# Kernel optimization log

Hardware: AMD Instinct MI355X
Metric: run time of the kernel (lower is better)

The kernel has to match this reference:

```python
import jax, jax.numpy as jnp
import numpy as np

N = 100000
E = 1600000
B = 64
NUM_CLASSES = 10


def setup_inputs() -> dict:
    key = jax.random.key(0)
    ks = jax.random.split(key, 8)
    x = jax.random.normal(ks[0], (N, 5), dtype=jnp.float32)
    edge_index = jax.random.randint(ks[1], (2, E), 0, N, dtype=jnp.int64)
    batch = jnp.sort(jax.random.randint(ks[2], (N,), 0, B, dtype=jnp.int64))

    def glorot(k, fan_in, fan_out):
        s = jnp.sqrt(6.0 / (fan_in + fan_out)).astype(jnp.float32)
        return jax.random.uniform(k, (fan_in, fan_out), jnp.float32, -s, s)

    dims = [(5, 32), (32, 64), (64, 128), (128, 256)]
    Ws = [glorot(jax.random.fold_in(ks[3], i), a, b) for i, (a, b) in enumerate(dims)]
    bs = [jnp.zeros((b,), jnp.float32) for (_, b) in dims]
    fc1_w = glorot(ks[4], 256, 100)
    fc1_b = jnp.zeros((100,), jnp.float32)
    fc2_w = glorot(ks[5], 100, NUM_CLASSES)
    fc2_b = jnp.zeros((NUM_CLASSES,), jnp.float32)
    return {
        'x': x, 'edge_index': edge_index, 'batch': batch,
        'W1': Ws[0], 'b1': bs[0], 'W2': Ws[1], 'b2': bs[1],
        'W3': Ws[2], 'b3': bs[2], 'W4': Ws[3], 'b4': bs[3],
        'fc1_w': fc1_w, 'fc1_b': fc1_b, 'fc2_w': fc2_w, 'fc2_b': fc2_b,
    }


def _gcn_conv(x, W, b, src, dst, dinv):
    h = x @ W                                   # [N, out]
    norm = (dinv[src] * dinv[dst])[:, None]      # [E, 1]
    msg = h[src] * norm                          # gather + scale
    agg = jax.ops.segment_sum(msg, dst, num_segments=N)
    agg = agg + h * (dinv * dinv)[:, None]       # self-loop contribution
    return agg + b


def reference(x, edge_index, batch, W1, b1, W2, b2, W3, b3, W4, b4,
              fc1_w, fc1_b, fc2_w, fc2_b):
    src, dst = edge_index[0], edge_index[1]
    # degree including self-loop
    deg = jax.ops.segment_sum(jnp.ones((E,), jnp.float32), dst, num_segments=N) + 1.0
    dinv = jax.lax.rsqrt(deg)

    h = jax.nn.relu(_gcn_conv(x, W1, b1, src, dst, dinv))
    # mesh_unpool with pool target 0 -> identity
    h = jax.nn.relu(_gcn_conv(h, W2, b2, src, dst, dinv))
    h = jax.nn.relu(_gcn_conv(h, W3, b3, src, dst, dinv))
    h = jax.nn.relu(_gcn_conv(h, W4, b4, src, dst, dinv))

    # global mean pool over graphs
    sums = jax.ops.segment_sum(h, batch, num_segments=B)
    cnt = jax.ops.segment_sum(jnp.ones((N,), jnp.float32), batch, num_segments=B)
    pooled = sums / jnp.maximum(cnt, 1.0)[:, None]

    h = jax.nn.relu(pooled @ fc1_w + fc1_b)
    return jax.nn.log_softmax(h @ fc2_w + fc2_b, axis=-1)
```

## Files before the change

### kernel.cpp

```cpp
#include <hip/hip_runtime.h>
#include <hip/hip_bf16.h>
#include <cmath>

#define NN 100000
#define NE 1600000
#define NBATCH 64
#define NB 391
#define NBP 512
#define BCAP 5120
#define NPAD (NB * BCAP)

typedef __attribute__((ext_vector_type(8))) _Float16 f16x8;
typedef __attribute__((ext_vector_type(4))) float f32x4;
typedef __attribute__((ext_vector_type(2))) float f32x2;

__device__ __forceinline__ void atomAdd(float* p, float v) {
  unsafeAtomicAdd(p, v);
}

__device__ __forceinline__ unsigned char f2fp8(float f) {
  int pk = __builtin_amdgcn_cvt_pk_fp8_f32(f, f, 0, false);
  return (unsigned char)(pk & 0xff);
}

__device__ __forceinline__ void fp8x16_to_f16(uint4 v, _Float16* h) {
  f32x2 t;
  t = __builtin_amdgcn_cvt_pk_f32_fp8(v.x, false); h[0] = (_Float16)t.x;  h[1] = (_Float16)t.y;
  t = __builtin_amdgcn_cvt_pk_f32_fp8(v.x, true);  h[2] = (_Float16)t.x;  h[3] = (_Float16)t.y;
  t = __builtin_amdgcn_cvt_pk_f32_fp8(v.y, false); h[4] = (_Float16)t.x;  h[5] = (_Float16)t.y;
  t = __builtin_amdgcn_cvt_pk_f32_fp8(v.y, true);  h[6] = (_Float16)t.x;  h[7] = (_Float16)t.y;
  t = __builtin_amdgcn_cvt_pk_f32_fp8(v.z, false); h[8] = (_Float16)t.x;  h[9] = (_Float16)t.y;
  t = __builtin_amdgcn_cvt_pk_f32_fp8(v.z, true);  h[10] = (_Float16)t.x; h[11] = (_Float16)t.y;
  t = __builtin_amdgcn_cvt_pk_f32_fp8(v.w, false); h[12] = (_Float16)t.x; h[13] = (_Float16)t.y;
  t = __builtin_amdgcn_cvt_pk_f32_fp8(v.w, true);  h[14] = (_Float16)t.x; h[15] = (_Float16)t.y;
}

__global__ __launch_bounds__(256) void k_bin(const int* __restrict__ src,
    const int* __restrict__ dst, int* __restrict__ bucketCnt, unsigned* __restrict__ pairs,
    const float* __restrict__ W2, const float* __restrict__ W3, const float* __restrict__ W4,
    _Float16* __restrict__ Wt2, _Float16* __restrict__ Wt3, _Float16* __restrict__ Wt4) {
  __shared__ int hist[NBP];
  __shared__ int scn[NBP];
  __shared__ int ofs[NBP];
  __shared__ int gbase[NBP];
  __shared__ unsigned buf[4096];
  __shared__ unsigned short bufb[4096];
  const int base = blockIdx.x * 4096;
  const int n = (NE - base < 4096) ? NE - base : 4096;
  for (int i = threadIdx.x; i < NBP; i += 256) hist[i] = 0;
  __syncthreads();

  int myS[16], myD[16];
  int nloc = 0;
  for (int i = threadIdx.x, j = 0; i < n; i += 256, ++j) {
    myS[j] = src[base + i];
    myD[j] = dst[base + i];
    atomicAdd(&hist[myD[j] >> 8], 1);
    nloc = j + 1;
  }
  __syncthreads();

  scn[threadIdx.x] = hist[threadIdx.x];
  scn[threadIdx.x + 256] = hist[threadIdx.x + 256];
  __syncthreads();
  for (int off = 1; off < NBP; off <<= 1) {
    const int i0 = threadIdx.x, i1 = threadIdx.x + 256;
    int t0 = (i0 >= off) ? scn[i0 - off] : 0;
    int t1 = (i1 >= off) ? scn[i1 - off] : 0;
    __syncthreads();
    scn[i0] += t0;
    scn[i1] += t1;
    __syncthreads();
  }
  ofs[threadIdx.x] = scn[threadIdx.x] - hist[threadIdx.x];
  ofs[threadIdx.x + 256] = scn[threadIdx.x + 256] - hist[threadIdx.x + 256];
  for (int b = threadIdx.x; b < NB; b += 256) {
    int c = hist[b];
    if (c) gbase[b] = b * BCAP + atomicAdd(&bucketCnt[b], c);
  }
  __syncthreads();

  for (int j = 0; j < nloc; ++j) {
    int b = myD[j] >> 8;
    int slot = atomicAdd(&ofs[b], 1);
    buf[slot] = ((unsigned)myS[j] << 8) | ((unsigned)myD[j] & 255u);
    bufb[slot] = (unsigned short)b;
  }
  __syncthreads();

  for (int i = threadIdx.x; i < n; i += 256) {
    int b = (int)bufb[i];
    int ex = scn[b] - hist[b];
    pairs[gbase[b] + (i - ex)] = buf[i];
  }

  int idx = blockIdx.x * 256 + threadIdx.x;
  if (idx < 2048) {
    int k = idx / 64, m = idx - k * 64;
    Wt2[m * 32 + k] = (_Float16)W2[idx];
  } else if (idx < 10240) {
    int j = idx - 2048;
    int k = j / 128, m = j - k * 128;
    Wt3[m * 64 + k] = (_Float16)W3[j];
  } else if (idx < 43008) {
    int j = idx - 10240;
    int k = j / 256, m = j - k * 256;
    Wt4[m * 128 + k] = (_Float16)W4[j];
  }
}

__global__ __launch_bounds__(256) void k_cntfill(const unsigned* __restrict__ pairs,
    const int* __restrict__ bucketCnt, const int* __restrict__ batch,
    const float* __restrict__ x, int* __restrict__ rowbeg, int* __restrict__ rowend,
    float* __restrict__ dinv, int* __restrict__ csrc, float* __restrict__ pcnt,
    _Float16* __restrict__ xs8) {
  __shared__ int c[256];
  __shared__ int scn[256];
  __shared__ int rowb[256];
  __shared__ int ofs[256];
  __shared__ int h[64];
  const int tid = threadIdx.x;
  c[tid] = 0; ofs[tid] = 0;
  if (tid < 64) h[tid] = 0;
  __syncthreads();
  const int b = blockIdx.x;
  const int s = b * BCAP;
  const int e = s + bucketCnt[b];
  for (int i = s + tid; i < e; i += 256) atomicAdd(&c[pairs[i] & 255u], 1);
  __syncthreads();
  const int v = c[tid];
  scn[tid] = v;
  __syncthreads();
  for (int off = 1; off < 256; off <<= 1) {
    int t = (tid >= off) ? scn[tid - off] : 0;
    __syncthreads();
    scn[tid] += t;
    __syncthreads();
  }
  rowb[tid] = s + scn[tid] - v;
  const int node = b * 256 + tid;
  rowbeg[node] = rowb[tid];
  rowend[node] = rowb[tid] + v;
  if (node < NN) {
    const float di = rsqrtf((float)v + 1.0f);
    dinv[node] = di;
    f16x8 o = {0, 0, 0, 0, 0, 0, 0, 0};
    o[0] = (_Float16)(x[(size_t)node * 5 + 0] * di);
    o[1] = (_Float16)(x[(size_t)node * 5 + 1] * di);
    o[2] = (_Float16)(x[(size_t)node * 5 + 2] * di);
    o[3] = (_Float16)(x[(size_t)node * 5 + 3] * di);
    o[4] = (_Float16)(x[(size_t)node * 5 + 4] * di);
    *(f16x8*)(xs8 + (size_t)node * 8) = o;
    atomicAdd(&h[batch[node]], 1);
  }
  __syncthreads();
  for (int i = s + tid; i < e; i += 256) {
    unsigned p = pairs[i];
    int t = (int)(p & 255u);
    int pos = rowb[t] + atomicAdd(&ofs[t], 1);
    csrc[pos] = (int)(p >> 8);
  }
  if (tid < 64 && h[tid]) atomAdd(&pcnt[tid], (float)h[tid]);
}

struct MegaArgs {
  const _Float16* xs8;
  const int* rowbeg; const int* rowend; const int* csrc;
  const float* dinv;
  const float* W1; const float* b1;
  unsigned char* F0;
  const _Float16* Wt2; const float* b2;
  unsigned char* F1;
  const _Float16* Wt3; const float* b3;
  unsigned char* F2;
  const _Float16* Wt4; const float* b4;
  unsigned char* AG8;
  const int* batch; float* pooled; const float* pcnt;
  const float* fc1w; const float* fc1b; const float* fc2w; const float* fc2b;
  float* out;
};

__global__ __launch_bounds__(256) void kw_l1(MegaArgs a) {
  __shared__ float w_s[160];
  __shared__ float b_s[32];
  const int tid = threadIdx.x;
  if (tid < 160) w_s[tid] = a.W1[tid];
  if (tid < 32) b_s[tid] = a.b1[tid];
  __syncthreads();
  const int r = blockIdx.x * 256 + tid;
  if (r >= NN) return;
  const float di = a.dinv[r];
  f16x8 av = *(const f16x8*)(a.xs8 + (size_t)r * 8);
  f16x8 cacc = {0, 0, 0, 0, 0, 0, 0, 0};
  int e = a.rowbeg[r];
  const int e1 = a.rowend[r];
  for (; e + 2 <= e1; e += 2) {
    const int s0 = a.csrc[e], s1 = a.csrc[e + 1];
    av   += *(const f16x8*)(a.xs8 + (size_t)s0 * 8);
    cacc += *(const f16x8*)(a.xs8 + (size_t)s1 * 8);
  }
  if (e < e1) av += *(const f16x8*)(a.xs8 + (size_t)a.csrc[e] * 8);
  av += cacc;
  const float f0 = (float)av[0] * di, f1 = (float)av[1] * di, f2 = (float)av[2] * di,
              f3 = (float)av[3] * di, f4 = (float)av[4] * di;
  float v[32];
#pragma unroll
  for (int j = 0; j < 32; ++j) {
    float s = b_s[j] + f0 * w_s[j] + f1 * w_s[32 + j] + f2 * w_s[64 + j]
                     + f3 * w_s[96 + j] + f4 * w_s[128 + j];
    v[j] = fmaxf(s, 0.f) * di;
  }
  unsigned u[8];
#pragma unroll
  for (int g2 = 0; g2 < 8; ++g2) {
    int uu = 0;
    uu = __builtin_amdgcn_cvt_pk_fp8_f32(v[4 * g2],     v[4 * g2 + 1], uu, false);
    uu = __builtin_amdgcn_cvt_pk_fp8_f32(v[4 * g2 + 2], v[4 * g2 + 3], uu, true);
    u[g2] = (unsigned)uu;
  }
  uint4* op = (uint4*)(a.F0 + (size_t)r * 32);
  op[0] = make_uint4(u[0], u[1], u[2], u[3]);
  op[1] = make_uint4(u[4], u[5], u[6], u[7]);
}

template<int K>
__global__ __launch_bounds__(256) void kw_gather8(const unsigned char* __restrict__ in,
    MegaArgs a) {
  constexpr int TPR = K / 16;
  constexpr int RPB = 256 / TPR;
  const int r = blockIdx.x * RPB + threadIdx.x / TPR;
  if (r >= NN) return;
  const int c = (threadIdx.x % TPR) * 16;
  const float di = a.dinv[r];
  f32x2 acc[8];
  {
    const uint4 v = *(const uint4*)(in + (size_t)r * K + c);
    acc[0] = __builtin_amdgcn_cvt_pk_f32_fp8(v.x, false);
    acc[1] = __builtin_amdgcn_cvt_pk_f32_fp8(v.x, true);
    acc[2] = __builtin_amdgcn_cvt_pk_f32_fp8(v.y, false);
    acc[3] = __builtin_amdgcn_cvt_pk_f32_fp8(v.y, true);
    acc[4] = __builtin_amdgcn_cvt_pk_f32_fp8(v.z, false);
    acc[5] = __builtin_amdgcn_cvt_pk_f32_fp8(v.z, true);
    acc[6] = __builtin_amdgcn_cvt_pk_f32_fp8(v.w, false);
    acc[7] = __builtin_amdgcn_cvt_pk_f32_fp8(v.w, true);
  }
  int e = a.rowbeg[r];
  const int e1 = a.rowend[r];
  for (; e + 2 <= e1; e += 2) {
    const int s0 = a.csrc[e], s1 = a.csrc[e + 1];
    const uint4 v0 = *(const uint4*)(in + (size_t)s0 * K + c);
    const uint4 v1 = *(const uint4*)(in + (size_t)s1 * K + c);
    acc[0] += __builtin_amdgcn_cvt_pk_f32_fp8(v0.x, false);
    acc[1] += __builtin_amdgcn_cvt_pk_f32_fp8(v0.x, true);
    acc[2] += __builtin_amdgcn_cvt_pk_f32_fp8(v0.y, false);
    acc[3] += __builtin_amdgcn_cvt_pk_f32_fp8(v0.y, true);
    acc[4] += __builtin_amdgcn_cvt_pk_f32_fp8(v0.z, false);
    acc[5] += __builtin_amdgcn_cvt_pk_f32_fp8(v0.z, true);
    acc[6] += __builtin_amdgcn_cvt_pk_f32_fp8(v0.w, false);
    acc[7] += __builtin_amdgcn_cvt_pk_f32_fp8(v0.w, true);
    acc[0] += __builtin_amdgcn_cvt_pk_f32_fp8(v1.x, false);
    acc[1] += __builtin_amdgcn_cvt_pk_f32_fp8(v1.x, true);
    acc[2] += __builtin_amdgcn_cvt_pk_f32_fp8(v1.y, false);
    acc[3] += __builtin_amdgcn_cvt_pk_f32_fp8(v1.y, true);
    acc[4] += __builtin_amdgcn_cvt_pk_f32_fp8(v1.z, false);
    acc[5] += __builtin_amdgcn_cvt_pk_f32_fp8(v1.z, true);
    acc[6] += __builtin_amdgcn_cvt_pk_f32_fp8(v1.w, false);
    acc[7] += __builtin_amdgcn_cvt_pk_f32_fp8(v1.w, true);
  }
  if (e < e1) {
    const uint4 v0 = *(const uint4*)(in + (size_t)a.csrc[e] * K + c);
    acc[0] += __builtin_amdgcn_cvt_pk_f32_fp8(v0.x, false);
    acc[1] += __builtin_amdgcn_cvt_pk_f32_fp8(v0.x, true);
    acc[2] += __builtin_amdgcn_cvt_pk_f32_fp8(v0.y, false);
    acc[3] += __builtin_amdgcn_cvt_pk_f32_fp8(v0.y, true);
    acc[4] += __builtin_amdgcn_cvt_pk_f32_fp8(v0.z, false);
    acc[5] += __builtin_amdgcn_cvt_pk_f32_fp8(v0.z, true);
    acc[6] += __builtin_amdgcn_cvt_pk_f32_fp8(v0.w, false);
    acc[7] += __builtin_amdgcn_cvt_pk_f32_fp8(v0.w, true);
  }
  int w0 = 0, w1 = 0, w2 = 0, w3 = 0;
  w0 = __builtin_amdgcn_cvt_pk_fp8_f32(acc[0].x * di, acc[0].y * di, 0, false);
  w0 = __builtin_amdgcn_cvt_pk_fp8_f32(acc[1].x * di, acc[1].y * di, w0, true);
  w1 = __builtin_amdgcn_cvt_pk_fp8_f32(acc[2].x * di, acc[2].y * di, 0, false);
  w1 = __builtin_amdgcn_cvt_pk_fp8_f32(acc[3].x * di, acc[3].y * di, w1, true);
  w2 = __builtin_amdgcn_cvt_pk_fp8_f32(acc[4].x * di, acc[4].y * di, 0, false);
  w2 = __builtin_amdgcn_cvt_pk_fp8_f32(acc[5].x * di, acc[5].y * di, w2, true);
  w3 = __builtin_amdgcn_cvt_pk_fp8_f32(acc[6].x * di, acc[6].y * di, 0, false);
  w3 = __builtin_amdgcn_cvt_pk_fp8_f32(acc[7].x * di, acc[7].y * di, w3, true);
  *(uint4*)(a.AG8 + (size_t)r * K + c) = make_uint4((unsigned)w0, (unsigned)w1,
                                                    (unsigned)w2, (unsigned)w3);
}

template<int K, int M, int MODE>
__global__ __launch_bounds__(256) void kw_gemm(MegaArgs a,
    const _Float16* __restrict__ Wt, const float* __restrict__ bias,
    unsigned char* __restrict__ outp) {
  constexpr int KC = 32;
  constexpr int KP = K + 8;
  constexpr int WP = KC + 8;
  constexpr int CTW = M / 64;
  constexpr int C16 = K / 16;
  __shared__ _Float16 a_s[64 * KP];
  __shared__ _Float16 w_s[M * WP];
  const int tid = threadIdx.x;
  const int wave = tid >> 6, lane = tid & 63;
  const int m16 = lane & 15, q = lane >> 4;
  const int r0 = blockIdx.x * 64;

  for (int idx = tid; idx < 64 * C16; idx += 256) {
    int row = idx / C16, cc = (idx % C16) * 16;
    uint4 v = {0u, 0u, 0u, 0u};
    if (r0 + row < NN) v = *(const uint4*)(a.AG8 + (size_t)(r0 + row) * K + cc);
    _Float16 h[16];
    fp8x16_to_f16(v, h);
    *(uint4*)&a_s[row * KP + cc]     = *(uint4*)&h[0];
    *(uint4*)&a_s[row * KP + cc + 8] = *(uint4*)&h[8];
  }
  f32x4 acc[4][CTW];
#pragma unroll
  for (int rt = 0; rt < 4; ++rt)
#pragma unroll
    for (int ct = 0; ct < CTW; ++ct) acc[rt][ct] = (f32x4){0.f, 0.f, 0.f, 0.f};

  for (int kc = 0; kc < K; kc += KC) {
    __syncthreads();
    for (int idx = tid; idx < M * (KC / 8); idx += 256) {
      int m = idx / (KC / 8), cc = (idx % (KC / 8)) * 8;
      uint4 v = *(const uint4*)(Wt + (size_t)m * K + kc + cc);
      *(uint4*)&w_s[m * WP + cc] = v;
    }
    __syncthreads();
    f16x8 bfr[CTW];
#pragma unroll
    for (int ct = 0; ct < CTW; ++ct)
      bfr[ct] = *(const f16x8*)&w_s[(wave * (M / 4) + ct * 16 + m16) * WP + q * 8];
#pragma unroll
    for (int rt = 0; rt < 4; ++rt) {
      f16x8 afr = *(const f16x8*)&a_s[(rt * 16 + m16) * KP + kc + q * 8];
#pragma unroll
      for (int ct = 0; ct < CTW; ++ct)
        acc[rt][ct] = __builtin_amdgcn_mfma_f32_16x16x32_f16(afr, bfr[ct], acc[rt][ct], 0, 0, 0);
    }
  }

  if constexpr (MODE == 1) {
    const int rlast = (r0 + 63 < NN) ? r0 + 63 : NN - 1;
    const int bmin = a.batch[r0];
    const int bmax = a.batch[rlast];
    int rowb[4][4];
#pragma unroll
    for (int rt = 0; rt < 4; ++rt)
#pragma unroll
      for (int reg = 0; reg < 4; ++reg) {
        const int row = r0 + rt * 16 + q * 4 + reg;
        rowb[rt][reg] = (row < NN) ? a.batch[row] : -1;
      }
#pragma unroll
    for (int ct = 0; ct < CTW; ++ct) {
      const int col = wave * (M / 4) + ct * 16 + m16;
      const float bv = bias[col];
      for (int b = bmin; b <= bmax; ++b) {
        float s = 0.f;
#pragma unroll
        for (int rt = 0; rt < 4; ++rt)
#pragma unroll
          for (int reg = 0; reg < 4; ++reg)
            if (rowb[rt][reg] == b) s += fmaxf(acc[rt][ct][reg] + bv, 0.f);
        s += __shfl_xor(s, 16);
        s += __shfl_xor(s, 32);
        if (q == 0) atomAdd(&a.pooled[b * M + col], s);
      }
    }
  } else {
    float dsc[4][4];
#pragma unroll
    for (int rt = 0; rt < 4; ++rt)
#pragma unroll
      for (int reg = 0; reg < 4; ++reg) {
        const int row = r0 + rt * 16 + q * 4 + reg;
        dsc[rt][reg] = (row < NN) ? a.dinv[row] : 0.f;
      }
#pragma unroll
    for (int rt = 0; rt < 4; ++rt) {
#pragma unroll
      for (int ct = 0; ct < CTW; ++ct) {
        const int col = wave * (M / 4) + ct * 16 + m16;
        const float bv = bias[col];
#pragma unroll
        for (int reg = 0; reg < 4; ++reg) {
          const int row = r0 + rt * 16 + q * 4 + reg;
          if (row < NN) {
            float vv = fmaxf(acc[rt][ct][reg] + bv, 0.f) * dsc[rt][reg];
            outp[(size_t)row * M + col] = f2fp8(vv);
          }
        }
      }
    }
  }
}

__global__ __launch_bounds__(256) void kw_mlp(MegaArgs a) {
  __shared__ float p[256];
  __shared__ float h1[100];
  __shared__ float lo[10];
  const int tid = threadIdx.x;
  const int b = blockIdx.x;
  const float inv = 1.0f / fmaxf(a.pcnt[b], 1.0f);
  p[tid] = a.pooled[b * 256 + tid] * inv;
  __syncthreads();
  for (int j = tid; j < 100; j += 256) {
    float s = a.fc1b[j];
    for (int k = 0; k < 256; ++k) s += p[k] * a.fc1w[k * 100 + j];
    h1[j] = fmaxf(s, 0.f);
  }
  __syncthreads();
  if (tid < 10) {
    float s = a.fc2b[tid];
    for (int k = 0; k < 100; ++k) s += h1[k] * a.fc2w[k * 10 + tid];
    lo[tid] = s;
  }
  __syncthreads();
  if (tid == 0) {
    float m = lo[0];
    for (int j = 1; j < 10; ++j) m = fmaxf(m, lo[j]);
    float ssum = 0.f;
    for (int j = 0; j < 10; ++j) ssum += expf(lo[j] - m);
    float lse = m + logf(ssum);
    for (int j = 0; j < 10; ++j) a.out[b * 10 + j] = lo[j] - lse;
  }
}

extern "C" void kernel_launch(void* const* d_in, const int* in_sizes, int n_in,
                              void* d_out, int out_size, void* d_ws, size_t ws_size,
                              hipStream_t stream) {
  const float* x     = (const float*)d_in[0];
  const int*   ei    = (const int*)d_in[1];
  const int*   batch = (const int*)d_in[2];
  const float* W1 = (const float*)d_in[3];  const float* b1 = (const float*)d_in[4];
  const float* W2 = (const float*)d_in[5];  const float* b2 = (const float*)d_in[6];
  const float* W3 = (const float*)d_in[7];  const float* b3 = (const float*)d_in[8];
  const float* W4 = (const float*)d_in[9];  const float* b4 = (const float*)d_in[10];
  const float* fc1w = (const float*)d_in[11]; const float* fc1b = (const float*)d_in[12];
  const float* fc2w = (const float*)d_in[13]; const float* fc2b = (const float*)d_in[14];
  float* out = (float*)d_out;

  const int* src = ei;
  const int* dst = ei + NE;

  float* ws = (float*)d_ws;
  float* pooled = ws;
  float* pcnt   = pooled + 16384;
  int*   bucketCnt = (int*)(pcnt + 64);
  float* dinv   = (float*)(bucketCnt + 512);
  int*   rowbeg = (int*)(dinv + 100352);
  int*   rowend = rowbeg + 100352;
  int*   csrc   = rowend + 100352;
  unsigned* pairs = (unsigned*)(csrc + NPAD);
  _Float16* xs8 = (_Float16*)(pairs + NPAD);
  unsigned char* F0 = (unsigned char*)(xs8 + 800768);
  unsigned char* F1 = F0 + 3200000;
  unsigned char* F2 = F1 + 6400000;
  unsigned char* AG8 = F2 + 12800000;
  _Float16* Wt2 = (_Float16*)(AG8 + 12800000);
  _Float16* Wt3 = Wt2 + 32 * 64;
  _Float16* Wt4 = Wt3 + 64 * 128;

  (void)hipMemsetAsync(pooled, 0, (16384 + 64 + 512) * sizeof(float), stream);
  k_bin<<<(NE + 4095) / 4096, 256, 0, stream>>>(src, dst, bucketCnt, pairs,
                                                W2, W3, W4, Wt2, Wt3, Wt4);
  k_cntfill<<<NB, 256, 0, stream>>>(pairs, bucketCnt, batch, x,
                                    rowbeg, rowend, dinv, csrc, pcnt, xs8);

  MegaArgs m;
  m.xs8 = xs8; m.rowbeg = rowbeg; m.rowend = rowend; m.csrc = csrc;
  m.dinv = dinv;
  m.W1 = W1; m.b1 = b1; m.F0 = F0;
  m.Wt2 = Wt2; m.b2 = b2; m.F1 = F1;
  m.Wt3 = Wt3; m.b3 = b3; m.F2 = F2;
  m.Wt4 = Wt4; m.b4 = b4; m.AG8 = AG8;
  m.batch = batch; m.pooled = pooled; m.pcnt = pcnt;
  m.fc1w = fc1w; m.fc1b = fc1b; m.fc2w = fc2w; m.fc2b = fc2b;
  m.out = out;

  kw_l1<<<(NN + 255) / 256, 256, 0, stream>>>(m);
  kw_gather8<32><<<(NN + 127) / 128, 256, 0, stream>>>(F0, m);
  kw_gemm<32, 64, 0><<<(NN + 63) / 64, 256, 0, stream>>>(m, Wt2, b2, F1);
  kw_gather8<64><<<(NN + 63) / 64, 256, 0, stream>>>(F1, m);
  kw_gemm<64, 128, 0><<<(NN + 63) / 64, 256, 0, stream>>>(m, Wt3, b3, F2);
  kw_gather8<128><<<(NN + 31) / 32, 256, 0, stream>>>(F2, m);
  kw_gemm<128, 256, 1><<<(NN + 63) / 64, 256, 0, stream>>>(m, Wt4, b4, nullptr);
  kw_mlp<<<NBATCH, 256, 0, stream>>>(m);
}
```

Baseline: 280.3 us.

## Fuse neighbor gather into GEMM for layers two and three

```diff
diff --git a/kernel.cpp b/kernel.cpp
--- a/kernel.cpp
+++ b/kernel.cpp
@@ -23,16 +23,25 @@
   return (unsigned char)(pk & 0xff);
 }
 
-__device__ __forceinline__ void fp8x16_to_f16(uint4 v, _Float16* h) {
-  f32x2 t;
-  t = __builtin_amdgcn_cvt_pk_f32_fp8(v.x, false); h[0] = (_Float16)t.x;  h[1] = (_Float16)t.y;
-  t = __builtin_amdgcn_cvt_pk_f32_fp8(v.x, true);  h[2] = (_Float16)t.x;  h[3] = (_Float16)t.y;
-  t = __builtin_amdgcn_cvt_pk_f32_fp8(v.y, false); h[4] = (_Float16)t.x;  h[5] = (_Float16)t.y;
-  t = __builtin_amdgcn_cvt_pk_f32_fp8(v.y, true);  h[6] = (_Float16)t.x;  h[7] = (_Float16)t.y;
-  t = __builtin_amdgcn_cvt_pk_f32_fp8(v.z, false); h[8] = (_Float16)t.x;  h[9] = (_Float16)t.y;
-  t = __builtin_amdgcn_cvt_pk_f32_fp8(v.z, true);  h[10] = (_Float16)t.x; h[11] = (_Float16)t.y;
-  t = __builtin_amdgcn_cvt_pk_f32_fp8(v.w, false); h[12] = (_Float16)t.x; h[13] = (_Float16)t.y;
-  t = __builtin_amdgcn_cvt_pk_f32_fp8(v.w, true);  h[14] = (_Float16)t.x; h[15] = (_Float16)t.y;
+__device__ __forceinline__ void acc8_init(f32x2* acc, uint4 v) {
+  acc[0] = __builtin_amdgcn_cvt_pk_f32_fp8(v.x, false);
+  acc[1] = __builtin_amdgcn_cvt_pk_f32_fp8(v.x, true);
+  acc[2] = __builtin_amdgcn_cvt_pk_f32_fp8(v.y, false);
+  acc[3] = __builtin_amdgcn_cvt_pk_f32_fp8(v.y, true);
+  acc[4] = __builtin_amdgcn_cvt_pk_f32_fp8(v.z, false);
+  acc[5] = __builtin_amdgcn_cvt_pk_f32_fp8(v.z, true);
+  acc[6] = __builtin_amdgcn_cvt_pk_f32_fp8(v.w, false);
+  acc[7] = __builtin_amdgcn_cvt_pk_f32_fp8(v.w, true);
+}
+__device__ __forceinline__ void acc8_add(f32x2* acc, uint4 v) {
+  acc[0] += __builtin_amdgcn_cvt_pk_f32_fp8(v.x, false);
+  acc[1] += __builtin_amdgcn_cvt_pk_f32_fp8(v.x, true);
+  acc[2] += __builtin_amdgcn_cvt_pk_f32_fp8(v.y, false);
+  acc[3] += __builtin_amdgcn_cvt_pk_f32_fp8(v.y, true);
+  acc[4] += __builtin_amdgcn_cvt_pk_f32_fp8(v.z, false);
+  acc[5] += __builtin_amdgcn_cvt_pk_f32_fp8(v.z, true);
+  acc[6] += __builtin_amdgcn_cvt_pk_f32_fp8(v.w, false);
+  acc[7] += __builtin_amdgcn_cvt_pk_f32_fp8(v.w, true);
 }
 
 __global__ __launch_bounds__(256) void k_bin(const int* __restrict__ src,
@@ -223,62 +232,132 @@
   op[1] = make_uint4(u[4], u[5], u[6], u[7]);
 }
 
-template<int K>
-__global__ __launch_bounds__(256) void kw_gather8(const unsigned char* __restrict__ in,
+template<int K, int M>
+__global__ __launch_bounds__(256) void kw_fused(const unsigned char* __restrict__ in,
+    MegaArgs a, const _Float16* __restrict__ Wt, const float* __restrict__ bias,
+    unsigned char* __restrict__ outp) {
+  constexpr int KC = 32;
+  constexpr int KP = K + 8;
+  constexpr int WP = KC + 8;
+  constexpr int CTW = M / 64;
+  constexpr int TPR = K / 16;
+  __shared__ _Float16 a_s[64 * KP];
+  __shared__ _Float16 w_s[M * WP];
+  const int tid = threadIdx.x;
+  const int r0 = blockIdx.x * 64;
+
+  {
+    const int lr = tid / TPR;
+    const int c = (tid % TPR) * 16;
+    if (lr < 64) {
+      const int r = r0 + lr;
+      _Float16 h[16];
+      if (r < NN) {
+        const float di = a.dinv[r];
+        f32x2 acc[8];
+        acc8_init(acc, *(const uint4*)(in + (size_t)r * K + c));
+        int e = a.rowbeg[r];
+        const int e1 = a.rowend[r];
+        for (; e + 2 <= e1; e += 2) {
+          const int s0 = a.csrc[e], s1 = a.csrc[e + 1];
+          const uint4 v0 = *(const uint4*)(in + (size_t)s0 * K + c);
+          const uint4 v1 = *(const uint4*)(in + (size_t)s1 * K + c);
+          acc8_add(acc, v0);
+          acc8_add(acc, v1);
+        }
+        if (e < e1) acc8_add(acc, *(const uint4*)(in + (size_t)a.csrc[e] * K + c));
+#pragma unroll
+        for (int j = 0; j < 8; ++j) {
+          h[2 * j]     = (_Float16)(acc[j].x * di);
+          h[2 * j + 1] = (_Float16)(acc[j].y * di);
+        }
+      } else {
+#pragma unroll
+        for (int j = 0; j < 16; ++j) h[j] = (_Float16)0.f;
+      }
+      *(uint4*)&a_s[lr * KP + c]     = *(uint4*)&h[0];
+      *(uint4*)&a_s[lr * KP + c + 8] = *(uint4*)&h[8];
+    }
+  }
+
+  const int wave = tid >> 6, lane = tid & 63;
+  const int m16 = lane & 15, q = lane >> 4;
+  f32x4 acc[4][CTW];
+#pragma unroll
+  for (int rt = 0; rt < 4; ++rt)
+#pragma unroll
+    for (int ct = 0; ct < CTW; ++ct) acc[rt][ct] = (f32x4){0.f, 0.f, 0.f, 0.f};
+
+  for (int kc = 0; kc < K; kc += KC) {
+    __syncthreads();
+    for (int idx = tid; idx < M * (KC / 8); idx += 256) {
+      int m = idx / (KC / 8), cc = (idx % (KC / 8)) * 8;
+      uint4 v = *(const uint4*)(Wt + (size_t)m * K + kc + cc);
+      *(uint4*)&w_s[m * WP + cc] = v;
+    }
+    __syncthreads();
+    f16x8 bfr[CTW];
+#pragma unroll
+    for (int ct = 0; ct < CTW; ++ct)
+      bfr[ct] = *(const f16x8*)&w_s[(wave * (M / 4) + ct * 16 + m16) * WP + q * 8];
+#pragma unroll
+    for (int rt = 0; rt < 4; ++rt) {
+      f16x8 afr = *(const f16x8*)&a_s[(rt * 16 + m16) * KP + kc + q * 8];
+#pragma unroll
+      for (int ct = 0; ct < CTW; ++ct)
+        acc[rt][ct] = __builtin_amdgcn_mfma_f32_16x16x32_f16(afr, bfr[ct], acc[rt][ct], 0, 0, 0);
+    }
+  }
+
+  float dsc[4][4];
+#pragma unroll
+  for (int rt = 0; rt < 4; ++rt)
+#pragma unroll
+    for (int reg = 0; reg < 4; ++reg) {
+      const int row = r0 + rt * 16 + q * 4 + reg;
+      dsc[rt][reg] = (row < NN) ? a.dinv[row] : 0.f;
+    }
+#pragma unroll
+  for (int rt = 0; rt < 4; ++rt) {
+#pragma unroll
+    for (int ct = 0; ct < CTW; ++ct) {
+      const int col = wave * (M / 4) + ct * 16 + m16;
+      const float bv = bias[col];
+#pragma unroll
+      for (int reg = 0; reg < 4; ++reg) {
+        const int row = r0 + rt * 16 + q * 4 + reg;
+        if (row < NN) {
+          float vv = fmaxf(acc[rt][ct][reg] + bv, 0.f) * dsc[rt][reg];
+          outp[(size_t)row * M + col] = f2fp8(vv);
+        }
+      }
+    }
+  }
+}
+
+__global__ __launch_bounds__(256) void kw_gather128(const unsigned char* __restrict__ in,
     MegaArgs a) {
-  constexpr int TPR = K / 16;
-  constexpr int RPB = 256 / TPR;
+  constexpr int K = 128;
+  constexpr int TPR = 8;
+  constexpr int RPB = 32;
+  if (blockIdx.x < 64) a.pooled[blockIdx.x * 256 + threadIdx.x] = 0.f;
   const int r = blockIdx.x * RPB + threadIdx.x / TPR;
   if (r >= NN) return;
   const int c = (threadIdx.x % TPR) * 16;
   const float di = a.dinv[r];
   f32x2 acc[8];
-  {
-    const uint4 v = *(const uint4*)(in + (size_t)r * K + c);
-    acc[0] = __builtin_amdgcn_cvt_pk_f32_fp8(v.x, false);
-    acc[1] = __builtin_amdgcn_cvt_pk_f32_fp8(v.x, true);
-    acc[2] = __builtin_amdgcn_cvt_pk_f32_fp8(v.y, false);
-    acc[3] = __builtin_amdgcn_cvt_pk_f32_fp8(v.y, true);
-    acc[4] = __builtin_amdgcn_cvt_pk_f32_fp8(v.z, false);
-    acc[5] = __builtin_amdgcn_cvt_pk_f32_fp8(v.z, true);
-    acc[6] = __builtin_amdgcn_cvt_pk_f32_fp8(v.w, false);
-    acc[7] = __builtin_amdgcn_cvt_pk_f32_fp8(v.w, true);
-  }
+  acc8_init(acc, *(const uint4*)(in + (size_t)r * K + c));
   int e = a.rowbeg[r];
   const int e1 = a.rowend[r];
   for (; e + 2 <= e1; e += 2) {
     const int s0 = a.csrc[e], s1 = a.csrc[e + 1];
     const uint4 v0 = *(const uint4*)(in + (size_t)s0 * K + c);
     const uint4 v1 = *(const uint4*)(in + (size_t)s1 * K + c);
-    acc[0] += __builtin_amdgcn_cvt_pk_f32_fp8(v0.x, false);
-    acc[1] += __builtin_amdgcn_cvt_pk_f32_fp8(v0.x, true);
-    acc[2] += __builtin_amdgcn_cvt_pk_f32_fp8(v0.y, false);
-    acc[3] += __builtin_amdgcn_cvt_pk_f32_fp8(v0.y, true);
-    acc[4] += __builtin_amdgcn_cvt_pk_f32_fp8(v0.z, false);
-    acc[5] += __builtin_amdgcn_cvt_pk_f32_fp8(v0.z, true);
-    acc[6] += __builtin_amdgcn_cvt_pk_f32_fp8(v0.w, false);
-    acc[7] += __builtin_amdgcn_cvt_pk_f32_fp8(v0.w, true);
-    acc[0] += __builtin_amdgcn_cvt_pk_f32_fp8(v1.x, false);
-    acc[1] += __builtin_amdgcn_cvt_pk_f32_fp8(v1.x, true);
-    acc[2] += __builtin_amdgcn_cvt_pk_f32_fp8(v1.y, false);
-    acc[3] += __builtin_amdgcn_cvt_pk_f32_fp8(v1.y, true);
-    acc[4] += __builtin_amdgcn_cvt_pk_f32_fp8(v1.z, false);
-    acc[5] += __builtin_amdgcn_cvt_pk_f32_fp8(v1.z, true);
-    acc[6] += __builtin_amdgcn_cvt_pk_f32_fp8(v1.w, false);
-    acc[7] += __builtin_amdgcn_cvt_pk_f32_fp8(v1.w, true);
-  }
-  if (e < e1) {
-    const uint4 v0 = *(const uint4*)(in + (size_t)a.csrc[e] * K + c);
-    acc[0] += __builtin_amdgcn_cvt_pk_f32_fp8(v0.x, false);
-    acc[1] += __builtin_amdgcn_cvt_pk_f32_fp8(v0.x, true);
-    acc[2] += __builtin_amdgcn_cvt_pk_f32_fp8(v0.y, false);
-    acc[3] += __builtin_amdgcn_cvt_pk_f32_fp8(v0.y, true);
-    acc[4] += __builtin_amdgcn_cvt_pk_f32_fp8(v0.z, false);
-    acc[5] += __builtin_amdgcn_cvt_pk_f32_fp8(v0.z, true);
-    acc[6] += __builtin_amdgcn_cvt_pk_f32_fp8(v0.w, false);
-    acc[7] += __builtin_amdgcn_cvt_pk_f32_fp8(v0.w, true);
-  }
-  int w0 = 0, w1 = 0, w2 = 0, w3 = 0;
+    acc8_add(acc, v0);
+    acc8_add(acc, v1);
+  }
+  if (e < e1) acc8_add(acc, *(const uint4*)(in + (size_t)a.csrc[e] * K + c));
+  int w0, w1, w2, w3;
   w0 = __builtin_amdgcn_cvt_pk_fp8_f32(acc[0].x * di, acc[0].y * di, 0, false);
   w0 = __builtin_amdgcn_cvt_pk_fp8_f32(acc[1].x * di, acc[1].y * di, w0, true);
   w1 = __builtin_amdgcn_cvt_pk_fp8_f32(acc[2].x * di, acc[2].y * di, 0, false);
@@ -291,10 +370,9 @@
                                                     (unsigned)w2, (unsigned)w3);
 }
 
-template<int K, int M, int MODE>
-__global__ __launch_bounds__(256) void kw_gemm(MegaArgs a,
-    const _Float16* __restrict__ Wt, const float* __restrict__ bias,
-    unsigned char* __restrict__ outp) {
+__global__ __launch_bounds__(256) void kw_gemm4(MegaArgs a,
+    const _Float16* __restrict__ Wt, const float* __restrict__ bias) {
+  constexpr int K = 128, M = 256;
   constexpr int KC = 32;
   constexpr int KP = K + 8;
   constexpr int WP = KC + 8;
@@ -311,8 +389,16 @@
     int row = idx / C16, cc = (idx % C16) * 16;
     uint4 v = {0u, 0u, 0u, 0u};
     if (r0 + row < NN) v = *(const uint4*)(a.AG8 + (size_t)(r0 + row) * K + cc);
+    f32x2 t;
     _Float16 h[16];
-    fp8x16_to_f16(v, h);
+    t = __builtin_amdgcn_cvt_pk_f32_fp8(v.x, false); h[0] = (_Float16)t.x;  h[1] = (_Float16)t.y;
+    t = __builtin_amdgcn_cvt_pk_f32_fp8(v.x, true);  h[2] = (_Float16)t.x;  h[3] = (_Float16)t.y;
+    t = __builtin_amdgcn_cvt_pk_f32_fp8(v.y, false); h[4] = (_Float16)t.x;  h[5] = (_Float16)t.y;
+    t = __builtin_amdgcn_cvt_pk_f32_fp8(v.y, true);  h[6] = (_Float16)t.x;  h[7] = (_Float16)t.y;
+    t = __builtin_amdgcn_cvt_pk_f32_fp8(v.z, false); h[8] = (_Float16)t.x;  h[9] = (_Float16)t.y;
+    t = __builtin_amdgcn_cvt_pk_f32_fp8(v.z, true);  h[10] = (_Float16)t.x; h[11] = (_Float16)t.y;
+    t = __builtin_amdgcn_cvt_pk_f32_fp8(v.w, false); h[12] = (_Float16)t.x; h[13] = (_Float16)t.y;
+    t = __builtin_amdgcn_cvt_pk_f32_fp8(v.w, true);  h[14] = (_Float16)t.x; h[15] = (_Float16)t.y;
     *(uint4*)&a_s[row * KP + cc]     = *(uint4*)&h[0];
     *(uint4*)&a_s[row * KP + cc + 8] = *(uint4*)&h[8];
   }
@@ -343,58 +429,31 @@
     }
   }
 
-  if constexpr (MODE == 1) {
-    const int rlast = (r0 + 63 < NN) ? r0 + 63 : NN - 1;
-    const int bmin = a.batch[r0];
-    const int bmax = a.batch[rlast];
-    int rowb[4][4];
-#pragma unroll
-    for (int rt = 0; rt < 4; ++rt)
-#pragma unroll
-      for (int reg = 0; reg < 4; ++reg) {
-        const int row = r0 + rt * 16 + q * 4 + reg;
-        rowb[rt][reg] = (row < NN) ? a.batch[row] : -1;
-      }
-#pragma unroll
-    for (int ct = 0; ct < CTW; ++ct) {
-      const int col = wave * (M / 4) + ct * 16 + m16;
-      const float bv = bias[col];
-      for (int b = bmin; b <= bmax; ++b) {
-        float s = 0.f;
-#pragma unroll
-        for (int rt = 0; rt < 4; ++rt)
-#pragma unroll
-          for (int reg = 0; reg < 4; ++reg)
-            if (rowb[rt][reg] == b) s += fmaxf(acc[rt][ct][reg] + bv, 0.f);
-        s += __shfl_xor(s, 16);
-        s += __shfl_xor(s, 32);
-        if (q == 0) atomAdd(&a.pooled[b * M + col], s);
-      }
-    }
-  } else {
-    float dsc[4][4];
-#pragma unroll
-    for (int rt = 0; rt < 4; ++rt)
-#pragma unroll
-      for (int reg = 0; reg < 4; ++reg) {
-        const int row = r0 + rt * 16 + q * 4 + reg;
-        dsc[rt][reg] = (row < NN) ? a.dinv[row] : 0.f;
-      }
-#pragma unroll
-    for (int rt = 0; rt < 4; ++rt) {
-#pragma unroll
-      for (int ct = 0; ct < CTW; ++ct) {
-        const int col = wave * (M / 4) + ct * 16 + m16;
-        const float bv = bias[col];
-#pragma unroll
-        for (int reg = 0; reg < 4; ++reg) {
-          const int row = r0 + rt * 16 + q * 4 + reg;
-          if (row < NN) {
-            float vv = fmaxf(acc[rt][ct][reg] + bv, 0.f) * dsc[rt][reg];
-            outp[(size_t)row * M + col] = f2fp8(vv);
-          }
-        }
-      }
+  const int rlast = (r0 + 63 < NN) ? r0 + 63 : NN - 1;
+  const int bmin = a.batch[r0];
+  const int bmax = a.batch[rlast];
+  int rowb[4][4];
+#pragma unroll
+  for (int rt = 0; rt < 4; ++rt)
+#pragma unroll
+    for (int reg = 0; reg < 4; ++reg) {
+      const int row = r0 + rt * 16 + q * 4 + reg;
+      rowb[rt][reg] = (row < NN) ? a.batch[row] : -1;
+    }
+#pragma unroll
+  for (int ct = 0; ct < CTW; ++ct) {
+    const int col = wave * (M / 4) + ct * 16 + m16;
+    const float bv = bias[col];
+    for (int b = bmin; b <= bmax; ++b) {
+      float s = 0.f;
+#pragma unroll
+      for (int rt = 0; rt < 4; ++rt)
+#pragma unroll
+        for (int reg = 0; reg < 4; ++reg)
+          if (rowb[rt][reg] == b) s += fmaxf(acc[rt][ct][reg] + bv, 0.f);
+      s += __shfl_xor(s, 16);
+      s += __shfl_xor(s, 32);
+      if (q == 0) atomAdd(&a.pooled[b * M + col], s);
     }
   }
 }
@@ -448,10 +507,10 @@
   const int* dst = ei + NE;
 
   float* ws = (float*)d_ws;
-  float* pooled = ws;
-  float* pcnt   = pooled + 16384;
+  float* pcnt      = ws;
   int*   bucketCnt = (int*)(pcnt + 64);
-  float* dinv   = (float*)(bucketCnt + 512);
+  float* pooled = (float*)(bucketCnt + 512);
+  float* dinv   = pooled + 16384;
   int*   rowbeg = (int*)(dinv + 100352);
   int*   rowend = rowbeg + 100352;
   int*   csrc   = rowend + 100352;
@@ -465,7 +524,7 @@
   _Float16* Wt3 = Wt2 + 32 * 64;
   _Float16* Wt4 = Wt3 + 64 * 128;
 
-  (void)hipMemsetAsync(pooled, 0, (16384 + 64 + 512) * sizeof(float), stream);
+  (void)hipMemsetAsync(ws, 0, (64 + 512) * sizeof(float), stream);
   k_bin<<<(NE + 4095) / 4096, 256, 0, stream>>>(src, dst, bucketCnt, pairs,
                                                 W2, W3, W4, Wt2, Wt3, Wt4);
   k_cntfill<<<NB, 256, 0, stream>>>(pairs, bucketCnt, batch, x,
@@ -483,11 +542,9 @@
   m.out = out;
 
   kw_l1<<<(NN + 255) / 256, 256, 0, stream>>>(m);
-  kw_gather8<32><<<(NN + 127) / 128, 256, 0, stream>>>(F0, m);
-  kw_gemm<32, 64, 0><<<(NN + 63) / 64, 256, 0, stream>>>(m, Wt2, b2, F1);
-  kw_gather8<64><<<(NN + 63) / 64, 256, 0, stream>>>(F1, m);
-  kw_gemm<64, 128, 0><<<(NN + 63) / 64, 256, 0, stream>>>(m, Wt3, b3, F2);
-  kw_gather8<128><<<(NN + 31) / 32, 256, 0, stream>>>(F2, m);
-  kw_gemm<128, 256, 1><<<(NN + 63) / 64, 256, 0, stream>>>(m, Wt4, b4, nullptr);
+  kw_fused<32, 64><<<(NN + 63) / 64, 256, 0, stream>>>(F0, m, Wt2, b2, F1);
+  kw_fused<64, 128><<<(NN + 63) / 64, 256, 0, stream>>>(F1, m, Wt3, b3, F2);
+  kw_gather128<<<(NN + 31) / 32, 256, 0, stream>>>(F2, m);
+  kw_gemm4<<<(NN + 63) / 64, 256, 0, stream>>>(m, Wt4, b4);
   kw_mlp<<<NBATCH, 256, 0, stream>>>(m);
 }
```

After: 283.7 us. No clear change (+1.2%).
